# Kernel tuning notes

Measured on AMD Instinct MI355X. Metric: run time of the kernel, lower is better.

The kernel has to match this reference:

```python
import jax, jax.numpy as jnp
import numpy as np

N, IN_F, OUT_F = 2048, 512, 512

def setup_inputs() -> dict:
    key = jax.random.key(0)
    kx, ka, kb = jax.random.split(key, 3)
    x = jax.random.uniform(kx, (N, IN_F), dtype=jnp.float32)          # inputs in [0,1]
    a = jax.random.uniform(ka, (OUT_F, IN_F), dtype=jnp.float32)      # weight in [0,1]
    b = jax.random.uniform(kb, (OUT_F,), dtype=jnp.float32)           # bias in [0,1]
    return {"x": x, "a": a, "b": b}

def reference(x, a, b):
    # Lukasiewicz / max-plus 'matmul':
    # y[n,o] = max(0, max_i(x[n,i] + a[o,i] - 1)), then max with bias b[o].
    inter = x[:, None, :] + a[None, :, :] - 1.0        # [N, out, in]
    y = jnp.maximum(jnp.max(inter, axis=-1), 0.0)      # [N, out]
    y = jnp.maximum(y, b[None, :])
    return y
```

## Files before the change

kernel.cpp:

```cpp
#include <hip/hip_runtime.h>
#include <cstdint>


#define TILE 64
#define BK   64
#define NROW 2048
#define NK   512
#define NCOL 512

__device__ __forceinline__ void async_load16(const float* g, float* l) {
  __builtin_amdgcn_global_load_lds(
      (const __attribute__((address_space(1))) void*)g,
      (__attribute__((address_space(3))) void*)l,
      16, 0, 0);
}

__global__ __launch_bounds__(256) void luka_kernel(
    const float* __restrict__ X, const float* __restrict__ A,
    const float* __restrict__ Bv, float* __restrict__ Y) {
  __shared__ float xs[2][TILE * BK];
  __shared__ float as[2][TILE * BK];

  const int tid  = threadIdx.x;
  const int wave = tid >> 6;
  const int tx   = tid & 15;
  const int ty   = tid >> 4;
  const int rowBase = blockIdx.y * TILE;
  const int colBase = blockIdx.x * TILE;

  uint32_t xoff[4], aoff[4];
#pragma unroll
  for (int r = 0; r < 4; ++r) {
    int row = ty * 4 + r;
    uint32_t m = (uint32_t)((row & 15) ^ (row >> 2));
    xoff[r] = (uint32_t)row * 256u + (m << 4);
  }
#pragma unroll
  for (int c = 0; c < 4; ++c) {
    int row = tx * 4 + c;
    uint32_t m = (uint32_t)((row & 15) ^ (row >> 2));
    aoff[c] = (uint32_t)row * 256u + (m << 4);
  }

  float acc[4][4];
#pragma unroll
  for (int r = 0; r < 4; ++r)
#pragma unroll
    for (int c = 0; c < 4; ++c) acc[r][c] = 0.0f;

  const int row0 = tid >> 4;
  const int sl   = tid & 15;

  auto stage = [&](int buf, int kt) {
#pragma unroll
    for (int j = 0; j < 4; ++j) {
      int row = row0 + j * 16;
      int m   = (row & 15) ^ (row >> 2);
      int kk  = ((sl ^ m) << 2);
      const float* gx = X + (size_t)(rowBase + row) * NK + kt * BK + kk;
      const float* ga = A + (size_t)(colBase + row) * NK + kt * BK + kk;
      async_load16(gx, &xs[buf][j * 1024 + wave * 256]);
      async_load16(ga, &as[buf][j * 1024 + wave * 256]);
    }
  };

  stage(0, 0);
  __syncthreads();

  int buf = 0;
#pragma unroll 1
  for (int kt = 0; kt < NK / BK; ++kt) {
    if (kt < NK / BK - 1) stage(buf ^ 1, kt + 1);

    const char* xb = (const char*)&xs[buf][0];
    const char* ab = (const char*)&as[buf][0];
#pragma unroll
    for (int s4 = 0; s4 < BK / 4; ++s4) {
      float4 xf[4], af[4];
#pragma unroll
      for (int r = 0; r < 4; ++r)
        xf[r] = *(const float4*)(xb + (xoff[r] ^ (uint32_t)(s4 << 4)));
#pragma unroll
      for (int c = 0; c < 4; ++c)
        af[c] = *(const float4*)(ab + (aoff[c] ^ (uint32_t)(s4 << 4)));
#pragma unroll
      for (int r = 0; r < 4; ++r) {
#pragma unroll
        for (int c = 0; c < 4; ++c) {
          float s0 = xf[r].x + af[c].x;
          float s1 = xf[r].y + af[c].y;
          float s2 = xf[r].z + af[c].z;
          float s3 = xf[r].w + af[c].w;
          float t  = fmaxf(fmaxf(s0, s1), s2);
          acc[r][c] = fmaxf(fmaxf(t, s3), acc[r][c]);
        }
      }
    }
    __syncthreads();
    buf ^= 1;
  }

  const float4 bv = *(const float4*)&Bv[colBase + tx * 4];
#pragma unroll
  for (int r = 0; r < 4; ++r) {
    float4 o;
    o.x = fmaxf(fmaxf(acc[r][0] - 1.0f, 0.0f), bv.x);
    o.y = fmaxf(fmaxf(acc[r][1] - 1.0f, 0.0f), bv.y);
    o.z = fmaxf(fmaxf(acc[r][2] - 1.0f, 0.0f), bv.z);
    o.w = fmaxf(fmaxf(acc[r][3] - 1.0f, 0.0f), bv.w);
    *(float4*)&Y[(size_t)(rowBase + ty * 4 + r) * NCOL + colBase + tx * 4] = o;
  }
}

extern "C" void kernel_launch(void* const* d_in, const int* in_sizes, int n_in,
                              void* d_out, int out_size, void* d_ws, size_t ws_size,
                              hipStream_t stream) {
  const float* X = (const float*)d_in[0];
  const float* A = (const float*)d_in[1];
  const float* B = (const float*)d_in[2];
  float* Y = (float*)d_out;
  dim3 grid(NCOL / TILE, NROW / TILE);
  luka_kernel<<<grid, dim3(256), 0, stream>>>(X, A, B, Y);
}
```

Measured before the change: 94.72 us.

## Split the K reduction across two blocks and combine with integer atomicMax

Splits the reduction dimension over a third grid dimension with two K-chunks per output tile, doubling the block count from 256 to 512 so more CUs are busy. Partial maxima are merged into the output through integer atomicMax, which is valid because every value is clamped to be non-negative, and the output is zeroed with a memset first. The inner max is also regrouped to shorten the dependency chain on the accumulator. The cost is an extra memset launch, atomic traffic on every output element, and half as many K iterations per block to amortise the pipeline prologue.

```diff
diff --git a/kernel.cpp b/kernel.cpp
--- a/kernel.cpp
+++ b/kernel.cpp
@@ -7,6 +7,10 @@
 #define NROW 2048
 #define NK   512
 #define NCOL 512
+#define KSPLIT 2
+#define NKT  (NK / BK / KSPLIT)
+
+typedef float f32x4 __attribute__((ext_vector_type(4)));
 
 __device__ __forceinline__ void async_load16(const float* g, float* l) {
   __builtin_amdgcn_global_load_lds(
@@ -20,26 +24,24 @@
     const float* __restrict__ Bv, float* __restrict__ Y) {
   __shared__ float xs[2][TILE * BK];
   __shared__ float as[2][TILE * BK];
-
   const int tid  = threadIdx.x;
   const int wave = tid >> 6;
   const int tx   = tid & 15;
   const int ty   = tid >> 4;
   const int rowBase = blockIdx.y * TILE;
   const int colBase = blockIdx.x * TILE;
+  const int ktBase  = blockIdx.z * NKT;
 
   uint32_t xoff[4], aoff[4];
 #pragma unroll
   for (int r = 0; r < 4; ++r) {
     int row = ty * 4 + r;
-    uint32_t m = (uint32_t)((row & 15) ^ (row >> 2));
-    xoff[r] = (uint32_t)row * 256u + (m << 4);
+    xoff[r] = (uint32_t)row * 256u + ((uint32_t)((row & 15) ^ (row >> 2)) << 4);
   }
 #pragma unroll
   for (int c = 0; c < 4; ++c) {
     int row = tx * 4 + c;
-    uint32_t m = (uint32_t)((row & 15) ^ (row >> 2));
-    aoff[c] = (uint32_t)row * 256u + (m << 4);
+    aoff[c] = (uint32_t)row * 256u + ((uint32_t)((row & 15) ^ (row >> 2)) << 4);
   }
 
   float acc[4][4];
@@ -64,35 +66,32 @@
     }
   };
 
-  stage(0, 0);
+  stage(0, ktBase);
   __syncthreads();
 
   int buf = 0;
 #pragma unroll 1
-  for (int kt = 0; kt < NK / BK; ++kt) {
-    if (kt < NK / BK - 1) stage(buf ^ 1, kt + 1);
+  for (int t = 0; t < NKT; ++t) {
+    if (t < NKT - 1) stage(buf ^ 1, ktBase + t + 1);
 
     const char* xb = (const char*)&xs[buf][0];
     const char* ab = (const char*)&as[buf][0];
 #pragma unroll
     for (int s4 = 0; s4 < BK / 4; ++s4) {
-      float4 xf[4], af[4];
+      f32x4 xf[4], af[4];
 #pragma unroll
       for (int r = 0; r < 4; ++r)
-        xf[r] = *(const float4*)(xb + (xoff[r] ^ (uint32_t)(s4 << 4)));
+        xf[r] = *(const f32x4*)(xb + (xoff[r] ^ (uint32_t)(s4 << 4)));
 #pragma unroll
       for (int c = 0; c < 4; ++c)
-        af[c] = *(const float4*)(ab + (aoff[c] ^ (uint32_t)(s4 << 4)));
+        af[c] = *(const f32x4*)(ab + (aoff[c] ^ (uint32_t)(s4 << 4)));
 #pragma unroll
       for (int r = 0; r < 4; ++r) {
 #pragma unroll
         for (int c = 0; c < 4; ++c) {
-          float s0 = xf[r].x + af[c].x;
-          float s1 = xf[r].y + af[c].y;
-          float s2 = xf[r].z + af[c].z;
-          float s3 = xf[r].w + af[c].w;
-          float t  = fmaxf(fmaxf(s0, s1), s2);
-          acc[r][c] = fmaxf(fmaxf(t, s3), acc[r][c]);
+          f32x4 s = xf[r] + af[c];
+          float t0 = fmaxf(fmaxf(s.x, s.y), acc[r][c]);
+          acc[r][c] = fmaxf(fmaxf(s.z, s.w), t0);
         }
       }
     }
@@ -100,15 +99,17 @@
     buf ^= 1;
   }
 
-  const float4 bv = *(const float4*)&Bv[colBase + tx * 4];
+  const f32x4 bv = *(const f32x4*)&Bv[colBase + tx * 4];
+  float bvv[4] = {bv.x, bv.y, bv.z, bv.w};
+  int* Yi = (int*)Y;
 #pragma unroll
   for (int r = 0; r < 4; ++r) {
-    float4 o;
-    o.x = fmaxf(fmaxf(acc[r][0] - 1.0f, 0.0f), bv.x);
-    o.y = fmaxf(fmaxf(acc[r][1] - 1.0f, 0.0f), bv.y);
-    o.z = fmaxf(fmaxf(acc[r][2] - 1.0f, 0.0f), bv.z);
-    o.w = fmaxf(fmaxf(acc[r][3] - 1.0f, 0.0f), bv.w);
-    *(float4*)&Y[(size_t)(rowBase + ty * 4 + r) * NCOL + colBase + tx * 4] = o;
+    int base = (rowBase + ty * 4 + r) * NCOL + colBase + tx * 4;
+#pragma unroll
+    for (int c = 0; c < 4; ++c) {
+      float t = fmaxf(fmaxf(acc[r][c] - 1.0f, bvv[c]), 0.0f);
+      atomicMax(&Yi[base + c], __float_as_int(t));
+    }
   }
 }
 
@@ -119,6 +120,7 @@
   const float* A = (const float*)d_in[1];
   const float* B = (const float*)d_in[2];
   float* Y = (float*)d_out;
-  dim3 grid(NCOL / TILE, NROW / TILE);
+  hipMemsetAsync(Y, 0, (size_t)out_size * sizeof(float), stream);
+  dim3 grid(NCOL / TILE, NROW / TILE, KSPLIT);
   luka_kernel<<<grid, dim3(256), 0, stream>>>(X, A, B, Y);
 }
```

Measured after the change: 98.91 us. 1.04x slower.
